# Kernel optimization log

Hardware: AMD Instinct MI355X
Metric: run time of the kernel (lower is better)

The kernel has to match this reference:

```python
import jax, jax.numpy as jnp
import numpy as np

N_WIRES = 5
TOTAL = 2 * N_WIRES          # query branch simulates 2*n_wires qubits
DIM = 1 << TOTAL             # 1024
ENC = 1 << N_WIRES           # 32 = token encoder output dim


def setup_inputs() -> dict:
    key = jax.random.key(0)
    ks = jax.random.split(key, 6)
    B, T, C = 4, 32, 512
    x = jax.random.normal(ks[0], (B, T, C), jnp.float32)
    W_tok = jax.random.normal(ks[1], (ENC, C), jnp.float32) * 0.05
    b_tok = jax.random.normal(ks[2], (ENC,), jnp.float32) * 0.05
    theta_rx0 = jax.random.normal(ks[3], (TOTAL,), jnp.float32)
    theta_ry0 = jax.random.normal(ks[4], (TOTAL,), jnp.float32)
    theta_ry1 = jax.random.normal(ks[5], (TOTAL,), jnp.float32)
    return {"x": x, "W_tok": W_tok, "b_tok": b_tok,
            "theta_rx0": theta_rx0, "theta_ry0": theta_ry0, "theta_ry1": theta_ry1}


def _rx_mat(t):
    c = jnp.cos(t / 2).astype(jnp.complex64)
    s = jnp.sin(t / 2).astype(jnp.complex64)
    return jnp.stack([jnp.stack([c, -1j * s]), jnp.stack([-1j * s, c])])


def _ry_mat(t):
    c = jnp.cos(t / 2).astype(jnp.complex64)
    s = jnp.sin(t / 2).astype(jnp.complex64)
    return jnp.stack([jnp.stack([c, -s]), jnp.stack([s, c])])


def _apply_1q(state, U, w):
    # state: (bsz, 2, 2, ..., 2); wire w lives on axis 1+w (wire 0 = MSB)
    s = jnp.tensordot(state, U, axes=((1 + w,), (1,)))  # gate axis moves to last
    return jnp.moveaxis(s, -1, 1 + w)


def _apply_cnot(state, c, t):
    s = jnp.moveaxis(state, (1 + c, 1 + t), (-2, -1))
    s = s.at[..., 1, :].set(s[..., 1, ::-1])  # flip target where control == 1
    return jnp.moveaxis(s, (-2, -1), (1 + c, 1 + t))


def reference(x, W_tok, b_tok, theta_rx0, theta_ry0, theta_ry1):
    B, T, C = x.shape
    # token encoding + L2 normalize  -> (B, T, 32)
    enc = x @ W_tok.T + b_tok
    enc = enc / jnp.linalg.norm(enc, axis=-1, keepdims=True)
    # all T*T pairwise outer products, flattened as a_idx*32 + b_idx  -> (B, T*T, 1024)
    pairs = jnp.einsum('bip,bjq->bijpq', enc, enc).reshape(B, T * T, DIM)
    pairs = pairs / jnp.linalg.norm(pairs, axis=-1, keepdims=True)
    state = pairs.astype(jnp.complex64).reshape((B * T * T,) + (2,) * TOTAL)
    # layer 1: RX then RY on every wire
    for j in range(TOTAL):
        state = _apply_1q(state, _rx_mat(theta_rx0[j]), j)
        state = _apply_1q(state, _ry_mat(theta_ry0[j]), j)
    # CNOT ring
    for j in range(TOTAL):
        state = _apply_cnot(state, j, (j + 1) % TOTAL)
    # layer 2: RY on every wire
    for j in range(TOTAL):
        state = _apply_1q(state, _ry_mat(theta_ry1[j]), j)
    return state.reshape(B, T * T, DIM)
```

## Files before the change

kernel.cpp:

```cpp
#include <hip/hip_runtime.h>
#include <hip/hip_bf16.h>


__device__ __forceinline__ float2 cmulf(float2 a, float2 b) {
    return make_float2(a.x * b.x - a.y * b.y, a.x * b.y + a.y * b.x);
}
__device__ __forceinline__ float2 caddf(float2 a, float2 b) {
    return make_float2(a.x + b.x, a.y + b.y);
}
__device__ __forceinline__ float2 shflx(float2 v, int mask) {
    return make_float2(__shfl_xor(v.x, mask, 64), __shfl_xor(v.y, mask, 64));
}

__global__ __launch_bounds__(256) void prep_kernel(const float* __restrict__ x,
                                                   const float* __restrict__ W,
                                                   const float* __restrict__ bt,
                                                   const float* __restrict__ rx0,
                                                   const float* __restrict__ ry0,
                                                   const float* __restrict__ ry1,
                                                   float2* __restrict__ U,
                                                   float2* __restrict__ V) {
    int row = blockIdx.x;
    int tid = threadIdx.x;
    int col = tid & 31;
    int seg = tid >> 5;
    const float* xs = x + (size_t)row * 512 + seg * 64;
    const float* ws = W + (size_t)col * 512 + seg * 64;
    float part_acc = 0.f;
#pragma unroll
    for (int k = 0; k < 64; ++k) part_acc += xs[k] * ws[k];
    __shared__ float part[8][32];
    __shared__ float e[32];
    part[seg][col] = part_acc;
    __syncthreads();
    if (tid < 32) {
        float sum = bt[tid];
#pragma unroll
        for (int g = 0; g < 8; ++g) sum += part[g][tid];
        float sq = sum * sum;
#pragma unroll
        for (int off = 1; off < 32; off <<= 1) sq += __shfl_xor(sq, off, 64);
        e[tid] = sum * (1.0f / sqrtf(sq));
    }
    __syncthreads();

    int side = tid >> 7;
    int s = (tid >> 6) & 1;
    int t = (tid >> 5) & 1;
    int p = tid & 31;
    int wb = side * 5;

    float2 c = make_float2(e[p], 0.f);

#pragma unroll
    for (int l = 0; l < 5; ++l) {
        float tx = rx0[wb + l] * 0.5f, ty = ry0[wb + l] * 0.5f;
        float cx = cosf(tx), sx = sinf(tx), cy = cosf(ty), sy = sinf(ty);
        int bit = 1 << (4 - l);
        float2 pr = shflx(c, bit);
        float2 g00 = make_float2(cy * cx,  sy * sx);
        float2 g01 = make_float2(-sy * cx, -cy * sx);
        float2 g10 = make_float2(sy * cx,  -cy * sx);
        float2 g11 = make_float2(cy * cx,  -sy * sx);
        c = ((p & bit) == 0) ? caddf(cmulf(g00, c), cmulf(g01, pr))
                             : caddf(cmulf(g10, pr), cmulf(g11, c));
    }

    if (side == 0) {
#pragma unroll
        for (int l = 0; l < 4; ++l) {
            int cb = 1 << (4 - l), tb = 1 << (3 - l);
            float2 pr = shflx(c, tb);
            if (p & cb) c = pr;
        }
        if ((p & 1) != s) c = make_float2(0.f, 0.f);
        { float2 pr = shflx(c, 16); if (t) c = pr; }
    } else {
        { float2 pr = shflx(c, 16); if (s) c = pr; }
#pragma unroll
        for (int l = 0; l < 4; ++l) {
            int cb = 1 << (4 - l), tb = 1 << (3 - l);
            float2 pr = shflx(c, tb);
            if (p & cb) c = pr;
        }
        if ((p & 1) != t) c = make_float2(0.f, 0.f);
    }

#pragma unroll
    for (int l = 0; l < 5; ++l) {
        float ty = ry1[wb + l] * 0.5f;
        float cy = cosf(ty), sy = sinf(ty);
        int bit = 1 << (4 - l);
        float2 pr = shflx(c, bit);
        c = ((p & bit) == 0)
              ? make_float2(cy * c.x - sy * pr.x, cy * c.y - sy * pr.y)
              : make_float2(sy * pr.x + cy * c.x, sy * pr.y + cy * c.y);
    }

    float2* dst = (side == 0) ? U : V;
    dst[(size_t)row * 128 + (s * 2 + t) * 32 + p] = c;
}

__global__ __launch_bounds__(256) void outer_kernel(const float2* __restrict__ U,
                                                    const float2* __restrict__ V,
                                                    float* __restrict__ out,
                                                    int complex_out) {
    int bx = blockIdx.x;
    int b = blockIdx.y;
    int i = bx >> 5, j = bx & 31;
    int tid = threadIdx.x;
    __shared__ float2 su[128];
    __shared__ float2 sv[128];
    if (tid < 128) su[tid] = U[(size_t)(b * 32 + i) * 128 + tid];
    else           sv[tid - 128] = V[(size_t)(b * 32 + j) * 128 + (tid - 128)];
    __syncthreads();

    int d0 = tid << 2;
    int p = d0 >> 5;
    int q0 = d0 & 31;
    float2 up0 = su[p], up1 = su[32 + p], up2 = su[64 + p], up3 = su[96 + p];

    float2 acc[4];
#pragma unroll
    for (int e = 0; e < 4; ++e) {
        int q = q0 + e;
        float2 v0 = sv[q], v1 = sv[32 + q], v2 = sv[64 + q], v3 = sv[96 + q];
        float2 a;
        a.x = up0.x * v0.x - up0.y * v0.y + up1.x * v1.x - up1.y * v1.y
            + up2.x * v2.x - up2.y * v2.y + up3.x * v3.x - up3.y * v3.y;
        a.y = up0.x * v0.y + up0.y * v0.x + up1.x * v1.y + up1.y * v1.x
            + up2.x * v2.y + up2.y * v2.x + up3.x * v3.y + up3.y * v3.x;
        acc[e] = a;
    }

    size_t pair = (size_t)b * 1024 + bx;
    if (complex_out) {
        float4* o = (float4*)(out + (pair * 1024 + d0) * 2);
        o[0] = make_float4(acc[0].x, acc[0].y, acc[1].x, acc[1].y);
        o[1] = make_float4(acc[2].x, acc[2].y, acc[3].x, acc[3].y);
    } else {
        float4* o = (float4*)(out + pair * 1024 + d0);
        o[0] = make_float4(acc[0].x, acc[1].x, acc[2].x, acc[3].x);
    }
}

extern "C" void kernel_launch(void* const* d_in, const int* in_sizes, int n_in,
                              void* d_out, int out_size, void* d_ws, size_t ws_size,
                              hipStream_t stream) {
    const float* x   = (const float*)d_in[0];
    const float* W   = (const float*)d_in[1];
    const float* bt  = (const float*)d_in[2];
    const float* rx0 = (const float*)d_in[3];
    const float* ry0 = (const float*)d_in[4];
    const float* ry1 = (const float*)d_in[5];

    float2* U = (float2*)d_ws;
    float2* V = U + 16384;

    prep_kernel<<<128, 256, 0, stream>>>(x, W, bt, rx0, ry0, ry1, U, V);

    int complex_out = (out_size > 4 * 1024 * 1024) ? 1 : 0;
    dim3 grid(1024, 4);
    outer_kernel<<<grid, 256, 0, stream>>>(U, V, (float*)d_out, complex_out);
}
```

Baseline: 79.62 us.

## Fuse token encoding and circuit prep into outer-product kernel with 4 pairs per block

Merges the prep kernel (token encoder, normalization, per-branch circuit) and the outer-product kernel into a single launch. Each block now handles one i token and four j tokens. It recomputes the encoder dot products for those five rows and the branch circuits in-block, then writes four output pairs. This removes one kernel launch and the workspace round-trip, at the cost of redundant encoder and circuit work across blocks and a longer serial prologue before the stores.

New measurement: 104.2 us. 30.9% more time.

```diff
diff --git a/kernel.cpp b/kernel.cpp
--- a/kernel.cpp
+++ b/kernel.cpp
@@ -12,46 +12,13 @@
     return make_float2(__shfl_xor(v.x, mask, 64), __shfl_xor(v.y, mask, 64));
 }
 
-__global__ __launch_bounds__(256) void prep_kernel(const float* __restrict__ x,
-                                                   const float* __restrict__ W,
-                                                   const float* __restrict__ bt,
-                                                   const float* __restrict__ rx0,
-                                                   const float* __restrict__ ry0,
-                                                   const float* __restrict__ ry1,
-                                                   float2* __restrict__ U,
-                                                   float2* __restrict__ V) {
-    int row = blockIdx.x;
-    int tid = threadIdx.x;
-    int col = tid & 31;
-    int seg = tid >> 5;
-    const float* xs = x + (size_t)row * 512 + seg * 64;
-    const float* ws = W + (size_t)col * 512 + seg * 64;
-    float part_acc = 0.f;
-#pragma unroll
-    for (int k = 0; k < 64; ++k) part_acc += xs[k] * ws[k];
-    __shared__ float part[8][32];
-    __shared__ float e[32];
-    part[seg][col] = part_acc;
-    __syncthreads();
-    if (tid < 32) {
-        float sum = bt[tid];
-#pragma unroll
-        for (int g = 0; g < 8; ++g) sum += part[g][tid];
-        float sq = sum * sum;
-#pragma unroll
-        for (int off = 1; off < 32; off <<= 1) sq += __shfl_xor(sq, off, 64);
-        e[tid] = sum * (1.0f / sqrtf(sq));
-    }
-    __syncthreads();
-
-    int side = tid >> 7;
-    int s = (tid >> 6) & 1;
-    int t = (tid >> 5) & 1;
-    int p = tid & 31;
+__device__ __forceinline__ float2 circuit_branch(int side, int s, int t, int p,
+                                                 float e_p,
+                                                 const float* __restrict__ rx0,
+                                                 const float* __restrict__ ry0,
+                                                 const float* __restrict__ ry1) {
     int wb = side * 5;
-
-    float2 c = make_float2(e[p], 0.f);
-
+    float2 c = make_float2(e_p, 0.f);
 #pragma unroll
     for (int l = 0; l < 5; ++l) {
         float tx = rx0[wb + l] * 0.5f, ty = ry0[wb + l] * 0.5f;
@@ -65,7 +32,6 @@
         c = ((p & bit) == 0) ? caddf(cmulf(g00, c), cmulf(g01, pr))
                              : caddf(cmulf(g10, pr), cmulf(g11, c));
     }
-
     if (side == 0) {
 #pragma unroll
         for (int l = 0; l < 4; ++l) {
@@ -85,7 +51,6 @@
         }
         if ((p & 1) != t) c = make_float2(0.f, 0.f);
     }
-
 #pragma unroll
     for (int l = 0; l < 5; ++l) {
         float ty = ry1[wb + l] * 0.5f;
@@ -96,51 +61,117 @@
               ? make_float2(cy * c.x - sy * pr.x, cy * c.y - sy * pr.y)
               : make_float2(sy * pr.x + cy * c.x, sy * pr.y + cy * c.y);
     }
-
-    float2* dst = (side == 0) ? U : V;
-    dst[(size_t)row * 128 + (s * 2 + t) * 32 + p] = c;
+    return c;
 }
 
-__global__ __launch_bounds__(256) void outer_kernel(const float2* __restrict__ U,
-                                                    const float2* __restrict__ V,
+__global__ __launch_bounds__(256) void fused_kernel(const float* __restrict__ x,
+                                                    const float* __restrict__ W,
+                                                    const float* __restrict__ bt,
+                                                    const float* __restrict__ rx0,
+                                                    const float* __restrict__ ry0,
+                                                    const float* __restrict__ ry1,
                                                     float* __restrict__ out,
                                                     int complex_out) {
     int bx = blockIdx.x;
-    int b = blockIdx.y;
-    int i = bx >> 5, j = bx & 31;
+    int b  = bx >> 8;
+    int i  = (bx >> 3) & 31;
+    int j0 = (bx & 7) * 4;
     int tid = threadIdx.x;
+
+    __shared__ float part[5][8][32];
+    __shared__ float e[5][32];
     __shared__ float2 su[128];
-    __shared__ float2 sv[128];
-    if (tid < 128) su[tid] = U[(size_t)(b * 32 + i) * 128 + tid];
-    else           sv[tid - 128] = V[(size_t)(b * 32 + j) * 128 + (tid - 128)];
+    __shared__ float2 sv[4][128];
+
+    {
+        int col = tid & 31;
+        int seg = tid >> 5;
+        const float4* ws = (const float4*)(W + (size_t)col * 512 + seg * 64);
+        const float4* xr[5];
+        int rowi = b * 32 + i;
+        xr[0] = (const float4*)(x + (size_t)rowi * 512 + seg * 64);
+#pragma unroll
+        for (int v = 1; v < 5; ++v) {
+            int row = b * 32 + j0 + (v - 1);
+            xr[v] = (const float4*)(x + (size_t)row * 512 + seg * 64);
+        }
+        float acc[5] = {0.f, 0.f, 0.f, 0.f, 0.f};
+#pragma unroll
+        for (int k = 0; k < 16; ++k) {
+            float4 wv = ws[k];
+#pragma unroll
+            for (int v = 0; v < 5; ++v) {
+                float4 xv = xr[v][k];
+                acc[v] += xv.x * wv.x + xv.y * wv.y + xv.z * wv.z + xv.w * wv.w;
+            }
+        }
+#pragma unroll
+        for (int v = 0; v < 5; ++v) part[v][seg][col] = acc[v];
+    }
+    __syncthreads();
+
+    if (tid < 160) {
+        int v = tid >> 5, col = tid & 31;
+        float sum = bt[col];
+#pragma unroll
+        for (int g = 0; g < 8; ++g) sum += part[v][g][col];
+        float sq = sum * sum;
+#pragma unroll
+        for (int off = 1; off < 32; off <<= 1) sq += __shfl_xor(sq, off, 64);
+        e[v][col] = sum * (1.0f / sqrtf(sq));
+    }
+    __syncthreads();
+
+    {
+        int wavepair = tid >> 7;
+        int br = (tid >> 5) & 3;
+        int s = br >> 1, t = br & 1;
+        int p = tid & 31;
+        if (wavepair == 0) {
+            su[br * 32 + p]    = circuit_branch(0, s, t, p, e[0][p], rx0, ry0, ry1);
+        } else {
+            sv[0][br * 32 + p] = circuit_branch(1, s, t, p, e[1][p], rx0, ry0, ry1);
+        }
+        if (wavepair == 0) {
+            sv[1][br * 32 + p] = circuit_branch(1, s, t, p, e[2][p], rx0, ry0, ry1);
+        } else {
+            sv[2][br * 32 + p] = circuit_branch(1, s, t, p, e[3][p], rx0, ry0, ry1);
+        }
+        if (wavepair == 0) {
+            sv[3][br * 32 + p] = circuit_branch(1, s, t, p, e[4][p], rx0, ry0, ry1);
+        }
+    }
     __syncthreads();
 
     int d0 = tid << 2;
-    int p = d0 >> 5;
+    int pp = d0 >> 5;
     int q0 = d0 & 31;
-    float2 up0 = su[p], up1 = su[32 + p], up2 = su[64 + p], up3 = su[96 + p];
+    float2 up0 = su[pp], up1 = su[32 + pp], up2 = su[64 + pp], up3 = su[96 + pp];
 
-    float2 acc[4];
 #pragma unroll
-    for (int e = 0; e < 4; ++e) {
-        int q = q0 + e;
-        float2 v0 = sv[q], v1 = sv[32 + q], v2 = sv[64 + q], v3 = sv[96 + q];
-        float2 a;
-        a.x = up0.x * v0.x - up0.y * v0.y + up1.x * v1.x - up1.y * v1.y
-            + up2.x * v2.x - up2.y * v2.y + up3.x * v3.x - up3.y * v3.y;
-        a.y = up0.x * v0.y + up0.y * v0.x + up1.x * v1.y + up1.y * v1.x
-            + up2.x * v2.y + up2.y * v2.x + up3.x * v3.y + up3.y * v3.x;
-        acc[e] = a;
-    }
-
-    size_t pair = (size_t)b * 1024 + bx;
-    if (complex_out) {
-        float4* o = (float4*)(out + (pair * 1024 + d0) * 2);
-        o[0] = make_float4(acc[0].x, acc[0].y, acc[1].x, acc[1].y);
-        o[1] = make_float4(acc[2].x, acc[2].y, acc[3].x, acc[3].y);
-    } else {
-        float4* o = (float4*)(out + pair * 1024 + d0);
-        o[0] = make_float4(acc[0].x, acc[1].x, acc[2].x, acc[3].x);
+    for (int jj = 0; jj < 4; ++jj) {
+        const float2* svj = sv[jj];
+        float2 acc[4];
+#pragma unroll
+        for (int ee = 0; ee < 4; ++ee) {
+            int q = q0 + ee;
+            float2 v0 = svj[q], v1 = svj[32 + q], v2 = svj[64 + q], v3 = svj[96 + q];
+            float2 a;
+            a.x = up0.x * v0.x - up0.y * v0.y + up1.x * v1.x - up1.y * v1.y
+                + up2.x * v2.x - up2.y * v2.y + up3.x * v3.x - up3.y * v3.y;
+            a.y = up0.x * v0.y + up0.y * v0.x + up1.x * v1.y + up1.y * v1.x
+                + up2.x * v2.y + up2.y * v2.x + up3.x * v3.y + up3.y * v3.x;
+            acc[ee] = a;
+        }
+        size_t pair = (size_t)b * 1024 + (size_t)i * 32 + (j0 + jj);
+        if (complex_out) {
+            float4* o = (float4*)(out + (pair * 1024 + d0) * 2);
+            o[0] = make_float4(acc[0].x, acc[0].y, acc[1].x, acc[1].y);
+            o[1] = make_float4(acc[2].x, acc[2].y, acc[3].x, acc[3].y);
+        } else {
+            float4* o = (float4*)(out + pair * 1024 + d0);
+            o[0] = make_float4(acc[0].x, acc[1].x, acc[2].x, acc[3].x);
+        }
     }
 }
 
@@ -154,12 +185,7 @@
     const float* ry0 = (const float*)d_in[4];
     const float* ry1 = (const float*)d_in[5];
 
-    float2* U = (float2*)d_ws;
-    float2* V = U + 16384;
-
-    prep_kernel<<<128, 256, 0, stream>>>(x, W, bt, rx0, ry0, ry1, U, V);
-
     int complex_out = (out_size > 4 * 1024 * 1024) ? 1 : 0;
-    dim3 grid(1024, 4);
-    outer_kernel<<<grid, 256, 0, stream>>>(U, V, (float*)d_out, complex_out);
+    fused_kernel<<<1024, 256, 0, stream>>>(x, W, bt, rx0, ry0, ry1,
+                                           (float*)d_out, complex_out);
 }
```
